# Optimization experiments

Measured on AMD Instinct MI355X. Metric: run time of the kernel, lower is better.

Reference implementation:

```python
import jax, jax.numpy as jnp
import numpy as np

NUM_HEADS = 2
D = 512
D_HID = 2048


def _layer_norm(x, g, b, eps):
    mu = jnp.mean(x, axis=-1, keepdims=True)
    var = jnp.var(x, axis=-1, keepdims=True)
    return (x - mu) * jax.lax.rsqrt(var + eps) * g + b


def _attn_block(Q, K, V, resnet, Wq, Wk, Wv, ln_g, ln_b, w1, w2, fln_g, fln_b):
    # Linear projections (torch Linear: x @ W.T), no bias
    q = Q @ Wq.T
    k = K @ Wk.T
    v = V @ Wv.T
    B, N, C = q.shape
    gs = C // NUM_HEADS  # group size per head
    # split channels into heads == reshape [B,N,H,gs] -> [B,H,N,gs]
    qh = q.reshape(B, N, NUM_HEADS, gs).transpose(0, 2, 1, 3)
    kh = k.reshape(B, K.shape[1], NUM_HEADS, gs).transpose(0, 2, 1, 3)
    vh = v.reshape(B, V.shape[1], NUM_HEADS, gs).transpose(0, 2, 1, 3)
    scores = jnp.einsum('bhqd,bhkd->bhqk', qh, kh) / jnp.sqrt(jnp.asarray(gs, q.dtype))
    attn = jax.nn.softmax(scores, axis=-1)
    out = jnp.einsum('bhqk,bhkd->bhqd', attn, vh)
    # concat heads back to channel dim
    out = out.transpose(0, 2, 1, 3).reshape(B, N, C)
    x = out + resnet
    x = _layer_norm(x, ln_g, ln_b, 1e-5)
    # FFN (dropout is identity in eval mode)
    residual = x
    y = jax.nn.relu(x @ w1.T) @ w2.T
    y = y + residual
    y = _layer_norm(y, fln_g, fln_b, 1e-6)
    return y


def setup_inputs() -> dict:
    key = jax.random.key(0)
    ks = jax.random.split(key, 16)
    B, N = 4, 2048
    Fm = jax.random.normal(ks[0], (B, N, D), dtype=jnp.float32)
    Fs = jax.random.normal(ks[1], (B, N, D), dtype=jnp.float32)
    Fq = jax.random.normal(ks[2], (B, N, D), dtype=jnp.float32)
    s = 0.02
    Wq = jax.random.normal(ks[3], (3, D, D), dtype=jnp.float32) * s
    Wk = jax.random.normal(ks[4], (3, D, D), dtype=jnp.float32) * s
    Wv = jax.random.normal(ks[5], (3, D, D), dtype=jnp.float32) * s
    ln_g = jnp.ones((3, D), dtype=jnp.float32)
    ln_b = jnp.zeros((3, D), dtype=jnp.float32)
    w1 = jax.random.normal(ks[6], (3, D_HID, D), dtype=jnp.float32) * s
    w2 = jax.random.normal(ks[7], (3, D, D_HID), dtype=jnp.float32) * s
    fln_g = jnp.ones((3, D), dtype=jnp.float32)
    fln_b = jnp.zeros((3, D), dtype=jnp.float32)
    return {"Fm": Fm, "Fs": Fs, "Fq": Fq, "Wq": Wq, "Wk": Wk, "Wv": Wv,
            "ln_g": ln_g, "ln_b": ln_b, "w1": w1, "w2": w2,
            "fln_g": fln_g, "fln_b": fln_b, "out_dim": 512}


def reference(Fm, Fs, Fq, Wq, Wk, Wv, ln_g, ln_b, w1, w2, fln_g, fln_b, out_dim):
    def blk(i, Q, K, V, resnet):
        return _attn_block(Q, K, V, resnet, Wq[i], Wk[i], Wv[i], ln_g[i], ln_b[i],
                           w1[i], w2[i], fln_g[i], fln_b[i])
    css = blk(0, Fs, Fs, Fm, Fm)
    cqq = blk(1, Fq, Fq, Fq, Fq)
    csq = blk(2, cqq, Fs, css, css)
    return csq
```

## Files before the change

### kernel.cpp

```cpp
#include <hip/hip_runtime.h>

typedef __bf16 bf16_t;
typedef __bf16 bf16x8 __attribute__((ext_vector_type(8)));
typedef float  f32x4  __attribute__((ext_vector_type(4)));

#define GAS __attribute__((address_space(1)))
#define LAS __attribute__((address_space(3)))

enum { EPI_BF16 = 0, EPI_RELU = 1 };

__global__ void probe_dtype(const unsigned* __restrict__ lng_bits, int* __restrict__ flag)
{
    *flag = (lng_bits[0] == 0x3F800000u) ? 0 : 1;
}

__global__ __launch_bounds__(256) void conv_any(
    const void* __restrict__ src, long elem_off, bf16_t* __restrict__ dst,
    const int* __restrict__ flag, int n8)
{
    int i = blockIdx.x * 256 + threadIdx.x;
    if (i >= n8) return;
    if (*flag == 0) {
        const float4* s = (const float4*)((const float*)src + elem_off);
        float4 a = s[i * 2], b = s[i * 2 + 1];
        bf16x8 o = { (bf16_t)a.x, (bf16_t)a.y, (bf16_t)a.z, (bf16_t)a.w,
                     (bf16_t)b.x, (bf16_t)b.y, (bf16_t)b.z, (bf16_t)b.w };
        ((bf16x8*)dst)[i] = o;
    } else {
        const uint4* s = (const uint4*)((const bf16_t*)src + elem_off);
        ((uint4*)dst)[i] = s[i];
    }
}

__global__ __launch_bounds__(256) void widen_ln(
    const void* __restrict__ src, float* __restrict__ dst,
    const int* __restrict__ flag, int n)
{
    int i = blockIdx.x * 256 + threadIdx.x;
    if (i >= n) return;
    dst[i] = (*flag == 0) ? ((const float*)src)[i]
                          : (float)((const bf16_t*)src)[i];
}

template<int EPI, int TMv, int TNv, bool MULTI>
__global__ __launch_bounds__(256) void gemm_bt(
    const bf16_t* __restrict__ A0, const bf16_t* __restrict__ A1, const bf16_t* __restrict__ A2,
    const bf16_t* __restrict__ B0, const bf16_t* __restrict__ B1, const bf16_t* __restrict__ B2,
    bf16_t* __restrict__ C0, bf16_t* __restrict__ C1, bf16_t* __restrict__ C2,
    int K, int lda, int ldb, int ldc,
    long sAb, long sAh, long sBb, long sBh, long sCb, long sCh,
    float scale)
{
    constexpr int MF = TMv / 32, NF = TNv / 32;
    __shared__ bf16_t As[2][TMv][32];
    __shared__ bf16_t Bs[2][TNv][32];

    const bf16_t* A; const bf16_t* B; bf16_t* C; long cOff = 0;
    if constexpr (MULTI) {
        const int z = blockIdx.z;
        A = (z == 0) ? A0 : (z == 1) ? A1 : A2;
        B = (z == 0) ? B0 : (z == 1) ? B1 : B2;
        C = (z == 0) ? C0 : (z == 1) ? C1 : C2;
    } else {
        const long zb = blockIdx.z >> 1, zh = blockIdx.z & 1;
        A = A0 + zb * sAb + zh * sAh;
        B = B0 + zb * sBb + zh * sBh;
        C = C0; cOff = zb * sCb + zh * sCh;
    }

    int m_t, n_t;
    {
        const int gx = gridDim.x, gy = gridDim.y;
        if ((gy & 7) == 0) {
            const int L = blockIdx.y * gx + blockIdx.x;
            const int band_h = gy >> 3;
            const int r = L >> 3;
            m_t = (L & 7) * band_h + (r % band_h);
            n_t = r / band_h;
        } else { m_t = blockIdx.y; n_t = blockIdx.x; }
    }
    const int n0 = n_t * TNv;
    const int m0 = m_t * TMv;

    const int tid  = threadIdx.x;
    const int wave = tid >> 6, lane = tid & 63;
    const int wm = (wave >> 1) * (TMv / 2);
    const int wn = (wave & 1) * (TNv / 2);
    const int lrow = lane & 15, lquad = lane >> 4;
    const int drow = lane >> 2;
    const int dcol = (lane & 3) * 8;

    f32x4 acc[MF][NF];
    #pragma unroll
    for (int i = 0; i < MF; i++)
        #pragma unroll
        for (int j = 0; j < NF; j++) acc[i][j] = (f32x4){0.f, 0.f, 0.f, 0.f};

    const bf16_t* aP = A + (long)(m0 + wave * (TMv / 4) + drow) * lda + dcol;
    const bf16_t* bP = B + (long)(n0 + wave * (TNv / 4) + drow) * ldb + dcol;
    bf16_t* asW = &As[0][wave * (TMv / 4)][0];
    bf16_t* bsW = &Bs[0][wave * (TNv / 4)][0];

    for (int kk = 0; kk < K; kk += 64) {
        __syncthreads();
        #pragma unroll
        for (int p = 0; p < 2; p++) {
            #pragma unroll
            for (int i = 0; i < TMv / 64; i++)
                __builtin_amdgcn_global_load_lds(
                    (GAS void*)(aP + p * 32 + (long)i * 16 * lda),
                    (LAS void*)(asW + p * TMv * 32 + i * 16 * 32), 16, 0, 0);
            #pragma unroll
            for (int i = 0; i < TNv / 64; i++)
                __builtin_amdgcn_global_load_lds(
                    (GAS void*)(bP + p * 32 + (long)i * 16 * ldb),
                    (LAS void*)(bsW + p * TNv * 32 + i * 16 * 32), 16, 0, 0);
        }
        aP += 64; bP += 64;
        __syncthreads();

        #pragma unroll
        for (int p = 0; p < 2; p++) {
            bf16x8 af[MF], bfr[NF];
            #pragma unroll
            for (int mi = 0; mi < MF; mi++)
                af[mi] = *(const bf16x8*)&As[p][wm + mi * 16 + lrow][lquad * 8];
            #pragma unroll
            for (int ni = 0; ni < NF; ni++)
                bfr[ni] = *(const bf16x8*)&Bs[p][wn + ni * 16 + lrow][lquad * 8];
            #pragma unroll
            for (int mi = 0; mi < MF; mi++)
                #pragma unroll
                for (int ni = 0; ni < NF; ni++)
                    acc[mi][ni] = __builtin_amdgcn_mfma_f32_16x16x32_bf16(
                        af[mi], bfr[ni], acc[mi][ni], 0, 0, 0);
        }
    }

    const int colB = n0 + wn + lrow;
    const int rowB = m0 + wm + lquad * 4;
    #pragma unroll
    for (int mi = 0; mi < MF; mi++)
        #pragma unroll
        for (int ni = 0; ni < NF; ni++)
            #pragma unroll
            for (int r = 0; r < 4; r++) {
                float v = acc[mi][ni][r] * scale;
                if (EPI == EPI_RELU) v = fmaxf(v, 0.f);
                C[cOff + (long)(rowB + mi * 16 + r) * ldc + colB + ni * 16] = (bf16_t)v;
            }
}

__global__ __launch_bounds__(256) void transpose_v(
    const bf16_t* __restrict__ v, bf16_t* __restrict__ vT)
{
    __shared__ bf16_t t[64][72];
    const int m0 = blockIdx.x * 64;
    const int c0 = blockIdx.y * 64;
    const int tid = threadIdx.x;
    const int rr = tid >> 3;
    const int cc = (tid & 7) * 8;
    #pragma unroll
    for (int i = 0; i < 2; i++) {
        int r = rr + i * 32;
        *(uint4*)&t[r][cc] = *(const uint4*)&v[(long)(m0 + r) * 512 + c0 + cc];
    }
    __syncthreads();
    const int b = m0 >> 11;
    #pragma unroll
    for (int i = 0; i < 2; i++) {
        int d  = rr + i * 32;
        int gc = c0 + d;
        int h  = gc >> 8, dd = gc & 255;
        int n  = (m0 & 2047) + cc;
        bf16x8 tmp;
        #pragma unroll
        for (int j = 0; j < 8; j++) tmp[j] = t[cc + j][d];
        *(bf16x8*)&vT[((long)(b * 2 + h) * 256 + dd) * 2048 + n] = tmp;
    }
}

__global__ __launch_bounds__(256) void softmax_rows(bf16_t* __restrict__ buf)
{
    const long base = (long)blockIdx.x * 2048;
    const int tid = threadIdx.x;
    const int wave = tid >> 6, lane = tid & 63;
    __shared__ float red[8];
    bf16x8 x = *(const bf16x8*)&buf[base + tid * 8];
    float v[8];
    float mx = -1e30f;
    #pragma unroll
    for (int j = 0; j < 8; j++) { v[j] = (float)x[j]; mx = fmaxf(mx, v[j]); }
    for (int off = 32; off; off >>= 1) mx = fmaxf(mx, __shfl_xor(mx, off));
    if (lane == 0) red[wave] = mx;
    __syncthreads();
    mx = fmaxf(fmaxf(red[0], red[1]), fmaxf(red[2], red[3]));
    float s = 0.f;
    #pragma unroll
    for (int j = 0; j < 8; j++) { v[j] = __expf(v[j] - mx); s += v[j]; }
    for (int off = 32; off; off >>= 1) s += __shfl_xor(s, off);
    if (lane == 0) red[4 + wave] = s;
    __syncthreads();
    s = red[4] + red[5] + red[6] + red[7];
    const float inv = 1.f / s;
    bf16x8 y;
    #pragma unroll
    for (int j = 0; j < 8; j++) y[j] = (bf16_t)(v[j] * inv);
    *(bf16x8*)&buf[base + tid * 8] = y;
}

template<typename OutT>
__global__ __launch_bounds__(256) void add_ln(
    const bf16_t* xin, const bf16_t* __restrict__ res,
    const float* __restrict__ g, const float* __restrict__ bias,
    OutT* out, float eps)
{
    const int wave = threadIdx.x >> 6, lane = threadIdx.x & 63;
    const long row = (long)blockIdx.x * 4 + wave;
    const long base = row * 512 + lane * 8;
    bf16x8 a8 = *(const bf16x8*)&xin[base];
    bf16x8 r8 = *(const bf16x8*)&res[base];
    float v[8];
    #pragma unroll
    for (int j = 0; j < 8; j++) v[j] = (float)a8[j] + (float)r8[j];
    float s = 0.f, s2 = 0.f;
    #pragma unroll
    for (int j = 0; j < 8; j++) { s += v[j]; s2 += v[j] * v[j]; }
    for (int off = 32; off; off >>= 1) { s += __shfl_xor(s, off); s2 += __shfl_xor(s2, off); }
    const float mu  = s * (1.f / 512.f);
    const float var = s2 * (1.f / 512.f) - mu * mu;
    const float rs  = rsqrtf(var + eps);
    const int c0 = lane * 8;
    float4 g0 = *(const float4*)&g[c0];
    float4 g1 = *(const float4*)&g[c0 + 4];
    float4 b0 = *(const float4*)&bias[c0];
    float4 b1 = *(const float4*)&bias[c0 + 4];
    float gv[8] = { g0.x, g0.y, g0.z, g0.w, g1.x, g1.y, g1.z, g1.w };
    float bv[8] = { b0.x, b0.y, b0.z, b0.w, b1.x, b1.y, b1.z, b1.w };
    #pragma unroll
    for (int j = 0; j < 8; j++)
        out[base + j] = (OutT)((v[j] - mu) * rs * gv[j] + bv[j]);
}

extern "C" void kernel_launch(void* const* d_in, const int* in_sizes, int n_in,
                              void* d_out, int out_size, void* d_ws, size_t ws_size,
                              hipStream_t stream)
{
    const void* Fm    = d_in[0];
    const void* Fs    = d_in[1];
    const void* Fq    = d_in[2];
    const void* Wq    = d_in[3];
    const void* Wk    = d_in[4];
    const void* Wv    = d_in[5];
    const void* ln_g  = d_in[6];
    const void* ln_b  = d_in[7];
    const void* w1    = d_in[8];
    const void* w2    = d_in[9];
    const void* fln_g = d_in[10];
    const void* fln_b = d_in[11];
    (void)in_sizes; (void)n_in; (void)out_size; (void)ws_size;

    char* ws = (char*)d_ws;
    size_t off = 0;
    auto take = [&](size_t bytes) {
        char* p = ws + off;
        off += (bytes + 255) & ~(size_t)255;
        return p;
    };
    const size_t NT = 8192ul * 512;

    int*    flag = (int*)take(256);
    float*  lnw  = (float*)take(4ul * 1536 * 4);
    bf16_t* Fm_b = (bf16_t*)take(NT * 2);
    bf16_t* Fs_b = (bf16_t*)take(NT * 2);
    bf16_t* Fq_b = (bf16_t*)take(NT * 2);
    bf16_t* wqb  = (bf16_t*)take(3ul * 512 * 512 * 2);
    bf16_t* wkb  = (bf16_t*)take(3ul * 512 * 512 * 2);
    bf16_t* wvb  = (bf16_t*)take(3ul * 512 * 512 * 2);
    bf16_t* w1b  = (bf16_t*)take(3ul * 2048 * 512 * 2);
    bf16_t* w2b  = (bf16_t*)take(3ul * 512 * 2048 * 2);
    bf16_t* q_b  = (bf16_t*)take(NT * 2);
    bf16_t* k_b  = (bf16_t*)take(NT * 2);
    char*   R_v  = take(NT * 2);
    char*   R_vt = take(NT * 2);
    char*   R_sc = take(8ul * 2048 * 2048 * 2);

    bf16_t* css = Fm_b;
    bf16_t* cqq = Fq_b;

    bf16_t* v_b = (bf16_t*)R_v;
    bf16_t* ao  = (bf16_t*)R_v;
    bf16_t* x_b = (bf16_t*)R_v;
    bf16_t* vT  = (bf16_t*)R_vt;
    bf16_t* y_b = (bf16_t*)R_vt;
    bf16_t* sc  = (bf16_t*)R_sc;
    bf16_t* h_b = (bf16_t*)R_sc;

    dim3 blk(256);
    probe_dtype<<<dim3(1), dim3(1), 0, stream>>>((const unsigned*)ln_g, flag);

    auto conv = [&](const void* s, long eoff, bf16_t* d, size_t n) {
        int n8 = (int)(n / 8);
        conv_any<<<dim3((n8 + 255) / 256), blk, 0, stream>>>(s, eoff, d, flag, n8);
    };
    conv(Fm, 0, Fm_b, NT);
    conv(Fs, 0, Fs_b, NT);
    conv(Fq, 0, Fq_b, NT);
    conv(Wq, 0, wqb, 3ul * 512 * 512);
    conv(Wk, 0, wkb, 3ul * 512 * 512);
    conv(Wv, 0, wvb, 3ul * 512 * 512);
    conv(w1, 0, w1b, 3ul * 2048 * 512);
    conv(w2, 0, w2b, 3ul * 512 * 2048);
    widen_ln<<<dim3(6), blk, 0, stream>>>(ln_g,  lnw,            flag, 1536);
    widen_ln<<<dim3(6), blk, 0, stream>>>(ln_b,  lnw + 1536,     flag, 1536);
    widen_ln<<<dim3(6), blk, 0, stream>>>(fln_g, lnw + 2 * 1536, flag, 1536);
    widen_ln<<<dim3(6), blk, 0, stream>>>(fln_b, lnw + 3 * 1536, flag, 1536);

    auto block = [&](const bf16_t* Q, const bf16_t* Kin, const bf16_t* V,
                     const bf16_t* res, int i, void* outp, bool out_f32) {
        const bf16_t* wqr = wqb + (size_t)i * 512 * 512;
        const bf16_t* wkr = wkb + (size_t)i * 512 * 512;
        const bf16_t* wvr = wvb + (size_t)i * 512 * 512;
        const bf16_t* w1r = w1b + (size_t)i * 2048 * 512;
        const bf16_t* w2r = w2b + (size_t)i * 512 * 2048;
        const float* g1 = lnw + i * 512;
        const float* b1 = lnw + 1536 + i * 512;
        const float* g2 = lnw + 2 * 1536 + i * 512;
        const float* b2 = lnw + 3 * 1536 + i * 512;

        gemm_bt<EPI_BF16, 64, 64, true><<<dim3(8, 128, 3), blk, 0, stream>>>(
            Q, Kin, V, wqr, wkr, wvr, q_b, k_b, v_b,
            512, 512, 512, 512, 0, 0, 0, 0, 0, 0, 1.f);
        transpose_v<<<dim3(128, 8, 1), blk, 0, stream>>>(v_b, vT);

        gemm_bt<EPI_BF16, 128, 128, false><<<dim3(16, 16, 8), blk, 0, stream>>>(
            q_b, nullptr, nullptr, k_b, nullptr, nullptr, sc, nullptr, nullptr,
            256, 512, 512, 2048,
            1048576L, 256L, 1048576L, 256L, 8388608L, 4194304L, 0.0625f);
        softmax_rows<<<dim3(16384), blk, 0, stream>>>(sc);
        gemm_bt<EPI_BF16, 64, 64, false><<<dim3(4, 32, 8), blk, 0, stream>>>(
            sc, nullptr, nullptr, vT, nullptr, nullptr, ao, nullptr, nullptr,
            2048, 2048, 2048, 512,
            8388608L, 4194304L, 1048576L, 524288L, 1048576L, 256L, 1.f);
        add_ln<bf16_t><<<dim3(2048), blk, 0, stream>>>(ao, res, g1, b1, x_b, 1e-5f);

        gemm_bt<EPI_RELU, 128, 128, false><<<dim3(16, 64, 1), blk, 0, stream>>>(
            x_b, nullptr, nullptr, w1r, nullptr, nullptr, h_b, nullptr, nullptr,
            512, 512, 512, 2048, 0, 0, 0, 0, 0, 0, 1.f);
        gemm_bt<EPI_BF16, 64, 64, false><<<dim3(8, 128, 1), blk, 0, stream>>>(
            h_b, nullptr, nullptr, w2r, nullptr, nullptr, y_b, nullptr, nullptr,
            2048, 2048, 2048, 512, 0, 0, 0, 0, 0, 0, 1.f);
        if (out_f32)
            add_ln<float><<<dim3(2048), blk, 0, stream>>>(
                y_b, x_b, g2, b2, (float*)outp, 1e-6f);
        else
            add_ln<bf16_t><<<dim3(2048), blk, 0, stream>>>(
                y_b, x_b, g2, b2, (bf16_t*)outp, 1e-6f);
    };

    block(Fs_b, Fs_b, Fm_b, Fm_b, 0, css, false);
    block(Fq_b, Fq_b, Fq_b, Fq_b, 1, cqq, false);
    block(cqq,  Fs_b, css,  css,  2, d_out, true);
}
```

Before: 731.3 us.

## Batch input conversion launches and enlarge GEMM M-tiles to 128x64

Result: faster. 702.9 us (-3.9%).

```diff
diff --git a/kernel.cpp b/kernel.cpp
--- a/kernel.cpp
+++ b/kernel.cpp
@@ -14,32 +14,37 @@
     *flag = (lng_bits[0] == 0x3F800000u) ? 0 : 1;
 }
 
-__global__ __launch_bounds__(256) void conv_any(
-    const void* __restrict__ src, long elem_off, bf16_t* __restrict__ dst,
+__global__ __launch_bounds__(256) void conv_any3(
+    const void* __restrict__ s0, const void* __restrict__ s1, const void* __restrict__ s2,
+    bf16_t* __restrict__ d0, bf16_t* __restrict__ d1, bf16_t* __restrict__ d2,
     const int* __restrict__ flag, int n8)
 {
     int i = blockIdx.x * 256 + threadIdx.x;
     if (i >= n8) return;
+    const void* src = (blockIdx.z == 0) ? s0 : (blockIdx.z == 1) ? s1 : s2;
+    bf16_t*    dst = (blockIdx.z == 0) ? d0 : (blockIdx.z == 1) ? d1 : d2;
     if (*flag == 0) {
-        const float4* s = (const float4*)((const float*)src + elem_off);
+        const float4* s = (const float4*)src;
         float4 a = s[i * 2], b = s[i * 2 + 1];
         bf16x8 o = { (bf16_t)a.x, (bf16_t)a.y, (bf16_t)a.z, (bf16_t)a.w,
                      (bf16_t)b.x, (bf16_t)b.y, (bf16_t)b.z, (bf16_t)b.w };
         ((bf16x8*)dst)[i] = o;
     } else {
-        const uint4* s = (const uint4*)((const bf16_t*)src + elem_off);
-        ((uint4*)dst)[i] = s[i];
-    }
-}
-
-__global__ __launch_bounds__(256) void widen_ln(
-    const void* __restrict__ src, float* __restrict__ dst,
-    const int* __restrict__ flag, int n)
+        ((uint4*)dst)[i] = ((const uint4*)src)[i];
+    }
+}
+
+__global__ __launch_bounds__(256) void widen_ln4(
+    const void* __restrict__ a, const void* __restrict__ b,
+    const void* __restrict__ c, const void* __restrict__ d,
+    float* __restrict__ dst, const int* __restrict__ flag, int n)
 {
     int i = blockIdx.x * 256 + threadIdx.x;
-    if (i >= n) return;
-    dst[i] = (*flag == 0) ? ((const float*)src)[i]
-                          : (float)((const bf16_t*)src)[i];
+    int seg = i / n, j = i - seg * n;
+    if (seg >= 4) return;
+    const void* s = (seg == 0) ? a : (seg == 1) ? b : (seg == 2) ? c : d;
+    dst[i] = (*flag == 0) ? ((const float*)s)[j]
+                          : (float)((const bf16_t*)s)[j];
 }
 
 template<int EPI, int TMv, int TNv, bool MULTI>
@@ -299,22 +304,13 @@
     dim3 blk(256);
     probe_dtype<<<dim3(1), dim3(1), 0, stream>>>((const unsigned*)ln_g, flag);
 
-    auto conv = [&](const void* s, long eoff, bf16_t* d, size_t n) {
-        int n8 = (int)(n / 8);
-        conv_any<<<dim3((n8 + 255) / 256), blk, 0, stream>>>(s, eoff, d, flag, n8);
-    };
-    conv(Fm, 0, Fm_b, NT);
-    conv(Fs, 0, Fs_b, NT);
-    conv(Fq, 0, Fq_b, NT);
-    conv(Wq, 0, wqb, 3ul * 512 * 512);
-    conv(Wk, 0, wkb, 3ul * 512 * 512);
-    conv(Wv, 0, wvb, 3ul * 512 * 512);
-    conv(w1, 0, w1b, 3ul * 2048 * 512);
-    conv(w2, 0, w2b, 3ul * 512 * 2048);
-    widen_ln<<<dim3(6), blk, 0, stream>>>(ln_g,  lnw,            flag, 1536);
-    widen_ln<<<dim3(6), blk, 0, stream>>>(ln_b,  lnw + 1536,     flag, 1536);
-    widen_ln<<<dim3(6), blk, 0, stream>>>(fln_g, lnw + 2 * 1536, flag, 1536);
-    widen_ln<<<dim3(6), blk, 0, stream>>>(fln_b, lnw + 3 * 1536, flag, 1536);
+    conv_any3<<<dim3(2048, 1, 3), blk, 0, stream>>>(
+        Fm, Fs, Fq, Fm_b, Fs_b, Fq_b, flag, (int)(NT / 8));
+    conv_any3<<<dim3(384, 1, 3), blk, 0, stream>>>(
+        Wq, Wk, Wv, wqb, wkb, wvb, flag, (int)(3ul * 512 * 512 / 8));
+    conv_any3<<<dim3(1536, 1, 2), blk, 0, stream>>>(
+        w1, w2, w2, w1b, w2b, w2b, flag, (int)(3ul * 2048 * 512 / 8));
+    widen_ln4<<<dim3(24), blk, 0, stream>>>(ln_g, ln_b, fln_g, fln_b, lnw, flag, 1536);
 
     auto block = [&](const bf16_t* Q, const bf16_t* Kin, const bf16_t* V,
                      const bf16_t* res, int i, void* outp, bool out_f32) {
@@ -328,7 +324,7 @@
         const float* g2 = lnw + 2 * 1536 + i * 512;
         const float* b2 = lnw + 3 * 1536 + i * 512;
 
-        gemm_bt<EPI_BF16, 64, 64, true><<<dim3(8, 128, 3), blk, 0, stream>>>(
+        gemm_bt<EPI_BF16, 128, 64, true><<<dim3(8, 64, 3), blk, 0, stream>>>(
             Q, Kin, V, wqr, wkr, wvr, q_b, k_b, v_b,
             512, 512, 512, 512, 0, 0, 0, 0, 0, 0, 1.f);
         transpose_v<<<dim3(128, 8, 1), blk, 0, stream>>>(v_b, vT);
@@ -338,7 +334,7 @@
             256, 512, 512, 2048,
             1048576L, 256L, 1048576L, 256L, 8388608L, 4194304L, 0.0625f);
         softmax_rows<<<dim3(16384), blk, 0, stream>>>(sc);
-        gemm_bt<EPI_BF16, 64, 64, false><<<dim3(4, 32, 8), blk, 0, stream>>>(
+        gemm_bt<EPI_BF16, 128, 64, false><<<dim3(4, 16, 8), blk, 0, stream>>>(
             sc, nullptr, nullptr, vT, nullptr, nullptr, ao, nullptr, nullptr,
             2048, 2048, 2048, 512,
             8388608L, 4194304L, 1048576L, 524288L, 1048576L, 256L, 1.f);
@@ -347,7 +343,7 @@
         gemm_bt<EPI_RELU, 128, 128, false><<<dim3(16, 64, 1), blk, 0, stream>>>(
             x_b, nullptr, nullptr, w1r, nullptr, nullptr, h_b, nullptr, nullptr,
             512, 512, 512, 2048, 0, 0, 0, 0, 0, 0, 1.f);
-        gemm_bt<EPI_BF16, 64, 64, false><<<dim3(8, 128, 1), blk, 0, stream>>>(
+        gemm_bt<EPI_BF16, 128, 64, false><<<dim3(8, 64, 1), blk, 0, stream>>>(
             h_b, nullptr, nullptr, w2r, nullptr, nullptr, y_b, nullptr, nullptr,
             2048, 2048, 2048, 512, 0, 0, 0, 0, 0, 0, 1.f);
         if (out_f32)
```
